# Performance work log

Hardware: AMD Instinct MI355X
Metric: run time of the kernel (lower is better)

The kernel has to match this reference:

```python
import jax, jax.numpy as jnp
import numpy as np

N_NODES = 100000
N_EDGES = 1600000
IN_DIM = 128
OUT_DIM = 128


def setup_inputs() -> dict:
    key = jax.random.key(0)
    k1, k2, k3, k4, k5 = jax.random.split(key, 5)
    x = jax.random.normal(k1, (N_NODES, IN_DIM), dtype=jnp.float32)
    edge_src = jax.random.randint(k2, (N_EDGES,), 0, N_NODES, dtype=jnp.int32)
    edge_dst = jax.random.randint(k3, (N_EDGES,), 0, N_NODES, dtype=jnp.int32)
    # nn.Linear(in_dim*2, out_dim): W stored here as [2*in_dim, out_dim] (already transposed)
    W = jax.random.normal(k4, (2 * IN_DIM, OUT_DIM), dtype=jnp.float32) * (1.0 / np.sqrt(2 * IN_DIM))
    b = jax.random.normal(k5, (OUT_DIM,), dtype=jnp.float32) * 0.01
    return {"x": x, "edge_src": edge_src, "edge_dst": edge_dst, "W": W, "b": b}


def reference(x, edge_src, edge_dst, W, b):
    # adj_mean @ x  ==  mean over neighbors: sum_j x[src_j] into row dst_j, / deg(dst)
    n = x.shape[0]
    deg = jax.ops.segment_sum(jnp.ones_like(edge_dst, dtype=x.dtype), edge_dst, num_segments=n)
    deg = jnp.maximum(deg, 1.0)  # rows with no neighbors -> zero vector (0/1)
    neigh = jax.ops.segment_sum(x[edge_src], edge_dst, num_segments=n) / deg[:, None]
    # concat([x, neigh], dim=1) then Linear
    out = jnp.concatenate([x, neigh], axis=1) @ W + b
    return out
```

## Files before the change

### kernel.cpp

```cpp
#include <hip/hip_runtime.h>

#define IN_DIM 128
#define OUT_DIM 128
#define PADCAP 1792
#define EPB 8192

typedef short bf16x8 __attribute__((ext_vector_type(8)));
typedef float f32x4 __attribute__((ext_vector_type(4)));
typedef float f32x2 __attribute__((ext_vector_type(2)));
typedef unsigned int u32x4 __attribute__((ext_vector_type(4)));

__device__ __forceinline__ unsigned short f2bf(float f) {
    union { float f; unsigned int u; } v; v.f = f;
    unsigned int u = v.u;
    u += 0x7FFFu + ((u >> 16) & 1u);
    return (unsigned short)(u >> 16);
}

__global__ __launch_bounds__(256) void prep_kernel(const float* __restrict__ x,
                                                   unsigned char* __restrict__ xq,
                                                   const float* __restrict__ W,
                                                   unsigned short* __restrict__ WF,
                                                   int* __restrict__ cursor,
                                                   int nN, int total8, int nconv, int nb) {
    const int b = blockIdx.x;
    const int t = threadIdx.x;
    if (b < nconv) {
        int i = b * 256 + t;
        if (i >= total8) return;
        const float4* p = (const float4*)x + (size_t)i * 2;
        float4 v0 = p[0], v1 = p[1];
        int w0 = 0, w1 = 0;
        w0 = __builtin_amdgcn_cvt_pk_fp8_f32(v0.x, v0.y, w0, false);
        w0 = __builtin_amdgcn_cvt_pk_fp8_f32(v0.z, v0.w, w0, true);
        w1 = __builtin_amdgcn_cvt_pk_fp8_f32(v1.x, v1.y, w1, false);
        w1 = __builtin_amdgcn_cvt_pk_fp8_f32(v1.z, v1.w, w1, true);
        uint2 o; o.x = (unsigned int)w0; o.y = (unsigned int)w1;
        int node = i >> 4, oct = i & 15;
        int q = oct >> 2, o8 = oct & 3;
        *(uint2*)(xq + (size_t)q * (nN + 1) * 32 + (size_t)node * 32 + o8 * 8) = o;
    } else if (b < nconv + 16) {
        int tt = (b - nconv) * 256 + t;
        int frag = tt >> 6, lane = tt & 63;
        int f = frag >> 3, c = frag & 7;
        int col = c * 16 + (lane & 15);
        int kbase = f * 32 + (lane >> 4) * 8;
        bf16x8 h;
#pragma unroll
        for (int i = 0; i < 8; i++)
            h[i] = (short)f2bf(W[(size_t)(kbase + i) * OUT_DIM + col]);
        *(bf16x8*)(WF + (size_t)tt * 8) = h;
    } else if (b == nconv + 16) {
        if (t < 32) {
            int q = t >> 3, o = t & 7;
            *(unsigned int*)(xq + (size_t)q * (nN + 1) * 32 + (size_t)nN * 32 + o * 4) = 0u;
        }
    } else {
        int i = (b - nconv - 17) * 256 + t;
        if (i < nb) cursor[i] = i * PADCAP;
    }
}

__global__ __launch_bounds__(1024) void place_kernel(const int* __restrict__ src,
                                                     const int* __restrict__ dst,
                                                     int* __restrict__ cursor,
                                                     unsigned int* __restrict__ csr_packed,
                                                     int nE, int nb) {
    __shared__ int lcnt[2048];
    __shared__ int lbase[2048];
    const int t = threadIdx.x;
    for (int i = t; i < nb; i += 1024) lcnt[i] = 0;
    __syncthreads();
    const int e0 = blockIdx.x * EPB;
    unsigned int meta[EPB / 1024];
#pragma unroll
    for (int k = 0; k < EPB / 1024; k++) {
        int e = e0 + k * 1024 + t;
        if (e < nE) {
            int d = dst[e];
            int bk = d >> 6, dl = d & 63;
            int r = atomicAdd(&lcnt[bk], 1);
            meta[k] = ((unsigned)bk << 20) | ((unsigned)dl << 14) | (unsigned)r;
        } else meta[k] = 0xFFFFFFFFu;
    }
    __syncthreads();
    for (int i = t; i < nb; i += 1024) {
        int c = lcnt[i];
        lbase[i] = c ? atomicAdd(&cursor[i], c) : 0;
    }
    __syncthreads();
#pragma unroll
    for (int k = 0; k < EPB / 1024; k++) {
        if (meta[k] != 0xFFFFFFFFu) {
            int e = e0 + k * 1024 + t;
            unsigned int m = meta[k];
            int bk = m >> 20, dl = (m >> 14) & 63, r = m & 0x3FFF;
            csr_packed[lbase[bk] + r] = ((unsigned)dl << 17) | (unsigned)src[e];
        }
    }
}

__global__ __launch_bounds__(256) void sort_kernel(unsigned int* __restrict__ csr_packed,
                                                   const int* __restrict__ cursor,
                                                   unsigned int* __restrict__ rowinfo,
                                                   int nN, int nb) {
    __shared__ int bcnt[64];
    __shared__ int bpst[64];
    __shared__ unsigned int sorted[PADCAP];
    const int b = blockIdx.x;
    const int t = threadIdx.x;
    const int lane = t & 63;
    const int wave = t >> 6;
    const size_t e0 = (size_t)b * PADCAP;
    int n = cursor[b] - (int)e0;
    if (n > PADCAP) n = PADCAP;

    const unsigned int sentinel = (unsigned)nN << 5;
    if (t < 64) bcnt[t] = 0;
#pragma unroll
    for (int k = 0; k < 7; k++) sorted[k * 256 + t] = sentinel;
    __syncthreads();

    unsigned int pk[7]; int rk[7];
#pragma unroll
    for (int k = 0; k < 7; k++) {
        int idx = k * 256 + t;
        if (idx < n) {
            unsigned int p = csr_packed[e0 + idx];
            pk[k] = p;
            rk[k] = atomicAdd(&bcnt[(p >> 17) & 63], 1);
        } else pk[k] = 0xFFFFFFFFu;
    }
    __syncthreads();

    if (wave == 0) {
        int dg = bcnt[lane];
        int pl = (dg + 7) & ~7;
        int s = pl;
#pragma unroll
        for (int off = 1; off < 64; off <<= 1) {
            int u = __shfl_up(s, off);
            if (lane >= off) s += u;
        }
        bpst[lane] = s - pl;
    }
    __syncthreads();

#pragma unroll
    for (int k = 0; k < 7; k++) {
        if (pk[k] != 0xFFFFFFFFu) {
            int dl = (pk[k] >> 17) & 63;
            sorted[bpst[dl] + rk[k]] = (pk[k] & 0x1FFFFu) << 5;
        }
    }
    __syncthreads();

#pragma unroll
    for (int k = 0; k < 7; k++) {
        int idx = k * 256 + t;
        csr_packed[e0 + idx] = sorted[idx];
    }
    if (t < 64) rowinfo[b * 64 + t] = (unsigned)bpst[t] | ((unsigned)bcnt[t] << 16);
}

__global__ __launch_bounds__(256, 8) void qgather_kernel(const unsigned char* __restrict__ xq,
                                                         const unsigned int* __restrict__ csr_packed,
                                                         const unsigned int* __restrict__ rowinfo,
                                                         unsigned short* __restrict__ neigh,
                                                         int nN, int nb) {
    __shared__ unsigned int el[PADCAP];
    __shared__ int bst[64];
    __shared__ int bdg[64];

    const int bid = blockIdx.x;
    const int xcd = bid & 7;
    const int quarter = xcd & 3;
    const int bucket = (bid >> 3) * 2 + (xcd >> 2);
    if (bucket >= nb) return;

    const int t = threadIdx.x;
    const int lane = t & 63;
    const int wave = t >> 6;

    if (t < 64) {
        unsigned int ri = rowinfo[bucket * 64 + t];
        bst[t] = (int)(ri & 0xFFFFu);
        bdg[t] = (int)(ri >> 16);
    }
    __syncthreads();
    const size_t e0 = (size_t)bucket * PADCAP;
    const int npad = bst[63] + ((bdg[63] + 7) & ~7);
    for (int idx = t; idx < npad; idx += 256) el[idx] = csr_packed[e0 + idx];
    __syncthreads();

    const int g = lane >> 2;
    const int c = lane & 3;
    const unsigned char* plane = xq + (size_t)quarter * (nN + 1) * 32 + c * 8;
    const int qoff = quarter * 32;

    const int r  = wave * 16 + g;
    const int st = bst[r];
    const int dg = bdg[r];
    const int pl = (dg + 7) & ~7;
    const unsigned int* ep = el + st;

    f32x2 a0{0.f, 0.f}, a1{0.f, 0.f}, a2{0.f, 0.f}, a3{0.f, 0.f};
    for (int j = 0; j < pl; j += 8) {
#pragma unroll
        for (int u = 0; u < 8; u++) {
            unsigned int s = ep[j + u];
            uint2 v = *(const uint2*)(plane + s);
            f32x2 p;
            p = __builtin_amdgcn_cvt_pk_f32_fp8(v.x, false); a0 += p;
            p = __builtin_amdgcn_cvt_pk_f32_fp8(v.x, true);  a1 += p;
            p = __builtin_amdgcn_cvt_pk_f32_fp8(v.y, false); a2 += p;
            p = __builtin_amdgcn_cvt_pk_f32_fp8(v.y, true);  a3 += p;
        }
    }
    const float rd = 1.0f / (float)((dg > 0) ? dg : 1);
    a0 *= rd; a1 *= rd; a2 *= rd; a3 *= rd;
    unsigned int w0, w1, w2, w3;
    asm("v_cvt_pk_bf16_f32 %0, %1, %2" : "=v"(w0) : "v"(a0.x), "v"(a0.y));
    asm("v_cvt_pk_bf16_f32 %0, %1, %2" : "=v"(w1) : "v"(a1.x), "v"(a1.y));
    asm("v_cvt_pk_bf16_f32 %0, %1, %2" : "=v"(w2) : "v"(a2.x), "v"(a2.y));
    asm("v_cvt_pk_bf16_f32 %0, %1, %2" : "=v"(w3) : "v"(a3.x), "v"(a3.y));
    u32x4 o = {w0, w1, w2, w3};
    const int row = bucket * 64 + r;
    *(u32x4*)(neigh + (size_t)row * IN_DIM + qoff + c * 8) = o;
}

__global__ __launch_bounds__(256, 6) void gemm_kernel(const float* __restrict__ x,
                                                      const unsigned short* __restrict__ neigh,
                                                      const unsigned short* __restrict__ WF,
                                                      const float* __restrict__ bias,
                                                      float* __restrict__ out, int nN) {
    const int t = threadIdx.x;
    const int lane = t & 63;
    const int wave = t >> 6;
    const int row0 = blockIdx.x * 64;

    f32x4 acc[8];
#pragma unroll
    for (int c = 0; c < 8; c++) acc[c] = f32x4{0.f, 0.f, 0.f, 0.f};

    const int arow = wave * 16 + (lane & 15);
    const int koff = (lane >> 4) * 8;
    const int rowc = min(row0 + arow, nN - 1);
    const float*          xrow = x     + (size_t)rowc * IN_DIM;
    const unsigned short* nrow = neigh + (size_t)rowc * IN_DIM;

#pragma unroll
    for (int f = 0; f < 8; f++) {
        bf16x8 af;
        if (f < 4) {
            const float* px = xrow + f * 32 + koff;
            float4 v0 = *(const float4*)px;
            float4 v1 = *(const float4*)(px + 4);
            unsigned int r0, r1, r2, r3;
            asm("v_cvt_pk_bf16_f32 %0, %1, %2" : "=v"(r0) : "v"(v0.x), "v"(v0.y));
            asm("v_cvt_pk_bf16_f32 %0, %1, %2" : "=v"(r1) : "v"(v0.z), "v"(v0.w));
            asm("v_cvt_pk_bf16_f32 %0, %1, %2" : "=v"(r2) : "v"(v1.x), "v"(v1.y));
            asm("v_cvt_pk_bf16_f32 %0, %1, %2" : "=v"(r3) : "v"(v1.z), "v"(v1.w));
            union { unsigned int u[4]; bf16x8 v; } cv;
            cv.u[0] = r0; cv.u[1] = r1; cv.u[2] = r2; cv.u[3] = r3;
            af = cv.v;
        } else {
            af = *(const bf16x8*)(nrow + (f - 4) * 32 + koff);
        }
#pragma unroll
        for (int c = 0; c < 8; c++) {
            bf16x8 bf = *(const bf16x8*)(WF + ((size_t)(f * 8 + c) * 64 + lane) * 8);
            acc[c] = __builtin_amdgcn_mfma_f32_16x16x32_bf16(af, bf, acc[c], 0, 0, 0);
        }
    }

    const int orow0 = row0 + wave * 16 + (lane >> 4) * 4;
    const int ocol  = lane & 15;
#pragma unroll
    for (int c = 0; c < 8; c++) {
        const float bv = bias[c * 16 + ocol];
#pragma unroll
        for (int r = 0; r < 4; r++) {
            int row = orow0 + r;
            if (row < nN)
                out[(size_t)row * OUT_DIM + c * 16 + ocol] = acc[c][r] + bv;
        }
    }
}

extern "C" void kernel_launch(void* const* d_in, const int* in_sizes, int n_in,
                              void* d_out, int out_size, void* d_ws, size_t ws_size,
                              hipStream_t stream) {
    const float* x        = (const float*)d_in[0];
    const int*   edge_src = (const int*)d_in[1];
    const int*   edge_dst = (const int*)d_in[2];
    const float* W        = (const float*)d_in[3];
    const float* bias     = (const float*)d_in[4];
    float* out = (float*)d_out;

    const int nN = in_sizes[0] / IN_DIM;
    const int nE = in_sizes[1];
    const int nb = (nN + 63) >> 6;

    int* cursor = (int*)d_ws;
    unsigned int* csr_packed = (unsigned int*)(cursor + 2048);
    unsigned int* rowinfo = csr_packed + (size_t)nb * PADCAP;
    unsigned char* xq = (unsigned char*)(rowinfo + (size_t)nb * 64);
    unsigned short* WF = (unsigned short*)(xq + (size_t)4 * (nN + 1) * 32);
    unsigned short* neigh = WF + 128 * 256;

    const int total8 = nN * IN_DIM / 8;
    const int nconv  = (total8 + 255) / 256;
    const int ninit  = (nb + 255) / 256;
    prep_kernel<<<nconv + 17 + ninit, 256, 0, stream>>>(x, xq, W, WF, cursor,
                                                        nN, total8, nconv, nb);

    const int eblk = (nE + EPB - 1) / EPB;
    place_kernel<<<eblk, 1024, 0, stream>>>(edge_src, edge_dst, cursor, csr_packed, nE, nb);
    sort_kernel<<<nb, 256, 0, stream>>>(csr_packed, cursor, rowinfo, nN, nb);

    const int nbp2 = (nb + 1) / 2;
    qgather_kernel<<<nbp2 * 8, 256, 0, stream>>>(xq, csr_packed, rowinfo, neigh, nN, nb);
    gemm_kernel<<<(nN + 63) / 64, 256, 0, stream>>>(x, neigh, WF, bias, out, nN);
}
```

Baseline: 110.5 us.

## Sort rows by degree within bucket to balance gather wave work

The sort kernel now runs a 64-lane bitonic sort of rows by degree, so rows of similar degree share a wave in the gather. It packs the original row id into rowinfo so outputs scatter to the right place. It also writes only the padded portion of the CSR and passes the padded count through cursor. Each 16-lane group in the gather now reads its edge list in a rotated order to spread LDS bank accesses. The aim is less divergence from uneven degrees within a wave, at the cost of a small sort and tighter bit-packing of rowinfo (start in 11 bits, degree in 10).

```diff
diff --git a/kernel.cpp b/kernel.cpp
--- a/kernel.cpp
+++ b/kernel.cpp
@@ -101,18 +101,19 @@
 }
 
 __global__ __launch_bounds__(256) void sort_kernel(unsigned int* __restrict__ csr_packed,
-                                                   const int* __restrict__ cursor,
+                                                   int* __restrict__ cursor,
                                                    unsigned int* __restrict__ rowinfo,
                                                    int nN, int nb) {
     __shared__ int bcnt[64];
     __shared__ int bpst[64];
+    __shared__ int s_npad;
     __shared__ unsigned int sorted[PADCAP];
     const int b = blockIdx.x;
     const int t = threadIdx.x;
     const int lane = t & 63;
     const int wave = t >> 6;
     const size_t e0 = (size_t)b * PADCAP;
-    int n = cursor[b] - (int)e0;
+    int n = cursor[b] - (int)(b * PADCAP);
     if (n > PADCAP) n = PADCAP;
 
     const unsigned int sentinel = (unsigned)nN << 5;
@@ -143,6 +144,23 @@
             if (lane >= off) s += u;
         }
         bpst[lane] = s - pl;
+        if (lane == 63) s_npad = s;
+        unsigned key = ((unsigned)dg << 6) | (unsigned)lane;
+#pragma unroll
+        for (int k = 2; k <= 64; k <<= 1) {
+#pragma unroll
+            for (int j = k >> 1; j > 0; j >>= 1) {
+                unsigned other = __shfl_xor(key, j);
+                bool lower = (lane & j) == 0;
+                bool asc   = (lane & k) == 0;
+                unsigned mn = min(key, other), mx = max(key, other);
+                key = (lower == asc) ? mn : mx;
+            }
+        }
+        int rowid = key & 63;
+        int deg2  = key >> 6;
+        rowinfo[b * 64 + lane] = (unsigned)bpst[rowid] | ((unsigned)deg2 << 11)
+                               | ((unsigned)rowid << 21);
     }
     __syncthreads();
 
@@ -155,22 +173,25 @@
     }
     __syncthreads();
 
+    const int npadtot = s_npad;
 #pragma unroll
     for (int k = 0; k < 7; k++) {
         int idx = k * 256 + t;
-        csr_packed[e0 + idx] = sorted[idx];
-    }
-    if (t < 64) rowinfo[b * 64 + t] = (unsigned)bpst[t] | ((unsigned)bcnt[t] << 16);
+        if (idx < npadtot) csr_packed[e0 + idx] = sorted[idx];
+    }
+    if (t == 0) cursor[b] = npadtot;
 }
 
 __global__ __launch_bounds__(256, 8) void qgather_kernel(const unsigned char* __restrict__ xq,
                                                          const unsigned int* __restrict__ csr_packed,
                                                          const unsigned int* __restrict__ rowinfo,
+                                                         const int* __restrict__ cursor,
                                                          unsigned short* __restrict__ neigh,
                                                          int nN, int nb) {
     __shared__ unsigned int el[PADCAP];
     __shared__ int bst[64];
     __shared__ int bdg[64];
+    __shared__ int brw[64];
 
     const int bid = blockIdx.x;
     const int xcd = bid & 7;
@@ -184,12 +205,13 @@
 
     if (t < 64) {
         unsigned int ri = rowinfo[bucket * 64 + t];
-        bst[t] = (int)(ri & 0xFFFFu);
-        bdg[t] = (int)(ri >> 16);
+        bst[t] = (int)(ri & 0x7FFu);
+        bdg[t] = (int)((ri >> 11) & 0x3FFu);
+        brw[t] = (int)((ri >> 21) & 63u);
     }
     __syncthreads();
     const size_t e0 = (size_t)bucket * PADCAP;
-    const int npad = bst[63] + ((bdg[63] + 7) & ~7);
+    const int npad = cursor[bucket];
     for (int idx = t; idx < npad; idx += 256) el[idx] = csr_packed[e0 + idx];
     __syncthreads();
 
@@ -208,7 +230,7 @@
     for (int j = 0; j < pl; j += 8) {
 #pragma unroll
         for (int u = 0; u < 8; u++) {
-            unsigned int s = ep[j + u];
+            unsigned int s = ep[j + ((u + g) & 7)];
             uint2 v = *(const uint2*)(plane + s);
             f32x2 p;
             p = __builtin_amdgcn_cvt_pk_f32_fp8(v.x, false); a0 += p;
@@ -225,7 +247,7 @@
     asm("v_cvt_pk_bf16_f32 %0, %1, %2" : "=v"(w2) : "v"(a2.x), "v"(a2.y));
     asm("v_cvt_pk_bf16_f32 %0, %1, %2" : "=v"(w3) : "v"(a3.x), "v"(a3.y));
     u32x4 o = {w0, w1, w2, w3};
-    const int row = bucket * 64 + r;
+    const int row = bucket * 64 + brw[r];
     *(u32x4*)(neigh + (size_t)row * IN_DIM + qoff + c * 8) = o;
 }
 
@@ -320,6 +342,6 @@
     sort_kernel<<<nb, 256, 0, stream>>>(csr_packed, cursor, rowinfo, nN, nb);
 
     const int nbp2 = (nb + 1) / 2;
-    qgather_kernel<<<nbp2 * 8, 256, 0, stream>>>(xq, csr_packed, rowinfo, neigh, nN, nb);
+    qgather_kernel<<<nbp2 * 8, 256, 0, stream>>>(xq, csr_packed, rowinfo, cursor, neigh, nN, nb);
     gemm_kernel<<<(nN + 63) / 64, 256, 0, stream>>>(x, neigh, WF, bias, out, nN);
 }
```

Measured after the change: 110.0 us. No clear change (-0.4%).
